# Kernel optimization log

Measured on AMD Instinct MI355X. Metric: run time of the kernel, lower is better.

## Reference

```python
import jax, jax.numpy as jnp
import numpy as np

IMAGE_SIZE = 224  # positional table has IMAGE_SIZE+1 rows
POS_D = 64        # per-coordinate embedding width; 4 coords -> 256 per bbox
OBJ_TYPE_NUM = 128
BATCH = 2048


def _positional_encoding(n_pos, d):
    # standard sinusoidal encoding, matching positional_encoding() in the repo
    pos = np.arange(n_pos, dtype=np.float32)[:, None]
    i = np.arange(d, dtype=np.float32)[None, :]
    angle = pos / np.power(10000.0, (2.0 * np.floor(i / 2.0)) / d)
    pe = np.where((np.arange(d) % 2) == 0, np.sin(angle), np.cos(angle))
    return jnp.asarray(pe, dtype=jnp.float32)


def setup_inputs() -> dict:
    key = jax.random.key(0)
    k1, k2 = jax.random.split(key)
    batch_fractional_bboxs = jax.random.uniform(
        k1, (BATCH, OBJ_TYPE_NUM, 4), dtype=jnp.float32)
    batch_obj_vecs = jax.random.randint(
        k2, (BATCH, OBJ_TYPE_NUM), 0, 2, dtype=jnp.int32)
    position_embedding_matrix = _positional_encoding(IMAGE_SIZE + 1, POS_D)
    return {
        "batch_fractional_bboxs": batch_fractional_bboxs,
        "batch_obj_vecs": batch_obj_vecs,
        "position_embedding_matrix": position_embedding_matrix,
    }


def reference(batch_fractional_bboxs, batch_obj_vecs, position_embedding_matrix):
    B, T, _ = batch_fractional_bboxs.shape  # [B, OBJ_TYPE_NUM, 4]
    D = position_embedding_matrix.shape[1]
    # idx = int(clamp(frac * IMAGE_SIZE, 0, IMAGE_SIZE))  (truncation toward 0)
    idx = jnp.clip(batch_fractional_bboxs * IMAGE_SIZE, 0.0, float(IMAGE_SIZE))
    idx = jax.lax.stop_gradient(idx).astype(jnp.int32)  # [B, T, 4]
    # gather per-coordinate embeddings and flatten: [B, T, 4, D] -> [B, T, 4*D]
    emb = position_embedding_matrix[idx].reshape(B, T, 4 * D)
    mask = (batch_obj_vecs == 1)[:, :, None]
    PoE = jnp.where(mask, emb, jnp.zeros((), dtype=emb.dtype))
    return PoE.reshape(B * T, 4 * D)  # dense buffer before sparse pack
```

## Files before the change

kernel.cpp:

```cpp
#include <hip/hip_runtime.h>


#define ROI_ROWS  (2048 * 128)
#define ROI_IMG   224.0f
#define RPW       4
#define NGROUPS   (ROI_ROWS / RPW)
#define BLOCKS    2048
#define TOTAL_WAVES (BLOCKS * 4)
#define ITERS     (NGROUPS / TOTAL_WAVES)

typedef float vfloat4 __attribute__((ext_vector_type(4)));

__global__ __launch_bounds__(256) void RoIBridge_kernel(
    const float* __restrict__ bboxs,
    const int*   __restrict__ objs,
    const float* __restrict__ table,
    vfloat4*     __restrict__ out)
{
    (void)table;
    const int gwave = blockIdx.x * 4 + (threadIdx.x >> 6);
    const int lane  = threadIdx.x & 63;
    const int c     = lane >> 4;
    const int d4    = lane & 15;

    const float L      = 0.41524101186092029f;
    const float INV2PI = 0.15915494309189535f;
    const float fi0 = (float)(d4 * 2);
    const float s0 = exp2f(-fi0 * L) * INV2PI;
    const float s1 = exp2f(-(fi0 + 1.0f) * L) * INV2PI;

    int   obj[RPW];
    float frac[RPW];
    int   row0 = gwave * RPW;

#pragma unroll
    for (int r = 0; r < RPW; ++r) {
        obj[r]  = objs[row0 + r];
        frac[r] = bboxs[((row0 + r) << 2) + c];
    }

    const vfloat4 z = (vfloat4){0.0f, 0.0f, 0.0f, 0.0f};

#pragma unroll
    for (int it = 0; it < ITERS; ++it) {
        const int nrow0 = row0 + TOTAL_WAVES * RPW;
        int   nobj[RPW];
        float nfrac[RPW];
        if (it < ITERS - 1) {
#pragma unroll
            for (int r = 0; r < RPW; ++r) {
                nobj[r]  = objs[nrow0 + r];
                nfrac[r] = bboxs[((nrow0 + r) << 2) + c];
            }
        }

#pragma unroll
        for (int r = 0; r < RPW; ++r) {
            float v = fminf(fmaxf(frac[r] * ROI_IMG, 0.0f), ROI_IMG);
            const float pos = (float)(int)v;
            const float r0 = __builtin_amdgcn_fractf(pos * s0);
            const float r1 = __builtin_amdgcn_fractf(pos * s1);
            vfloat4 e;
            e.x = __builtin_amdgcn_sinf(r0);
            e.y = __builtin_amdgcn_cosf(r0);
            e.z = __builtin_amdgcn_sinf(r1);
            e.w = __builtin_amdgcn_cosf(r1);
            out[(row0 + r) * 64 + lane] = (obj[r] == 1) ? e : z;
        }

        if (it < ITERS - 1) {
#pragma unroll
            for (int r = 0; r < RPW; ++r) {
                obj[r]  = nobj[r];
                frac[r] = nfrac[r];
            }
            row0 = nrow0;
        }
    }
}

extern "C" void kernel_launch(void* const* d_in, const int* in_sizes, int n_in,
                              void* d_out, int out_size, void* d_ws, size_t ws_size,
                              hipStream_t stream) {
    const float* bboxs = (const float*)d_in[0];
    const int*   objs  = (const int*)d_in[1];
    const float* table = (const float*)d_in[2];
    vfloat4* out = (vfloat4*)d_out;

    RoIBridge_kernel<<<BLOCKS, 256, 0, stream>>>(bboxs, objs, table, out);
}
```

Measured before the change: 262.0 us.

## Give each wave 32 contiguous rows with batched loads and ballot-based object mask

Each wave now handles 32 contiguous rows instead of 4-row groups strided across the grid. All 32 bbox coordinates are loaded up front, and the object flags are read once per wave and packed into a ballot mask rather than loaded per row per lane. A scheduling barrier keeps the loads ahead of the compute and store phase. The intent is fewer, more coalesced global loads and contiguous output writes. The cost is higher register pressure and no overlap between loads and compute inside a wave.

After: 264.6 us. Within noise of the previous version (+1.0%).

```diff
diff --git a/kernel.cpp b/kernel.cpp
--- a/kernel.cpp
+++ b/kernel.cpp
@@ -3,11 +3,9 @@
 
 #define ROI_ROWS  (2048 * 128)
 #define ROI_IMG   224.0f
-#define RPW       4
-#define NGROUPS   (ROI_ROWS / RPW)
+#define RPW_TOT   32
 #define BLOCKS    2048
-#define TOTAL_WAVES (BLOCKS * 4)
-#define ITERS     (NGROUPS / TOTAL_WAVES)
+#define WAVES     (BLOCKS * 4)
 
 typedef float vfloat4 __attribute__((ext_vector_type(4)));
 
@@ -29,53 +27,34 @@
     const float s0 = exp2f(-fi0 * L) * INV2PI;
     const float s1 = exp2f(-(fi0 + 1.0f) * L) * INV2PI;
 
-    int   obj[RPW];
-    float frac[RPW];
-    int   row0 = gwave * RPW;
+    const int rowbase = gwave * RPW_TOT;
 
+    const int j31 = lane & 31;
+    const unsigned long long omask = __ballot(objs[rowbase + j31] == 1);
+
+    float frac[RPW_TOT];
 #pragma unroll
-    for (int r = 0; r < RPW; ++r) {
-        obj[r]  = objs[row0 + r];
-        frac[r] = bboxs[((row0 + r) << 2) + c];
-    }
+    for (int j = 0; j < RPW_TOT; ++j)
+        frac[j] = bboxs[((rowbase + j) << 2) + c];
+
+    asm volatile("" ::: "memory");
+    __builtin_amdgcn_sched_barrier(0);
 
     const vfloat4 z = (vfloat4){0.0f, 0.0f, 0.0f, 0.0f};
 
 #pragma unroll
-    for (int it = 0; it < ITERS; ++it) {
-        const int nrow0 = row0 + TOTAL_WAVES * RPW;
-        int   nobj[RPW];
-        float nfrac[RPW];
-        if (it < ITERS - 1) {
-#pragma unroll
-            for (int r = 0; r < RPW; ++r) {
-                nobj[r]  = objs[nrow0 + r];
-                nfrac[r] = bboxs[((nrow0 + r) << 2) + c];
-            }
-        }
-
-#pragma unroll
-        for (int r = 0; r < RPW; ++r) {
-            float v = fminf(fmaxf(frac[r] * ROI_IMG, 0.0f), ROI_IMG);
-            const float pos = (float)(int)v;
-            const float r0 = __builtin_amdgcn_fractf(pos * s0);
-            const float r1 = __builtin_amdgcn_fractf(pos * s1);
-            vfloat4 e;
-            e.x = __builtin_amdgcn_sinf(r0);
-            e.y = __builtin_amdgcn_cosf(r0);
-            e.z = __builtin_amdgcn_sinf(r1);
-            e.w = __builtin_amdgcn_cosf(r1);
-            out[(row0 + r) * 64 + lane] = (obj[r] == 1) ? e : z;
-        }
-
-        if (it < ITERS - 1) {
-#pragma unroll
-            for (int r = 0; r < RPW; ++r) {
-                obj[r]  = nobj[r];
-                frac[r] = nfrac[r];
-            }
-            row0 = nrow0;
-        }
+    for (int j = 0; j < RPW_TOT; ++j) {
+        float v = fminf(fmaxf(frac[j] * ROI_IMG, 0.0f), ROI_IMG);
+        const float pos = (float)(int)v;
+        const float r0 = __builtin_amdgcn_fractf(pos * s0);
+        const float r1 = __builtin_amdgcn_fractf(pos * s1);
+        vfloat4 e;
+        e.x = __builtin_amdgcn_sinf(r0);
+        e.y = __builtin_amdgcn_cosf(r0);
+        e.z = __builtin_amdgcn_sinf(r1);
+        e.w = __builtin_amdgcn_cosf(r1);
+        const bool o = (omask >> j) & 1ull;
+        out[(rowbase + j) * 64 + lane] = o ? e : z;
     }
 }
 
```
